# Kernel optimization log

Measured on AMD Instinct MI355X. Metric: run time of the kernel, lower is better.

## Reference

```python
import jax, jax.numpy as jnp
import numpy as np

N_NODES = 100000


def _gcn_layer(x, src, dst, deg_inv_sqrt, W, b):
    # GCNConv: out = D^{-1/2} (A + I) D^{-1/2} X W + b  (symmetric norm, self-loops)
    xw = x @ W  # [N, out]
    norm = deg_inv_sqrt[src] * deg_inv_sqrt[dst]  # [E]
    msg = xw[src] * norm[:, None]  # [E, out] gathered messages
    agg = jax.ops.segment_sum(msg, dst, num_segments=N_NODES)
    # self-loop contribution: norm_ii = deg_inv_sqrt[i]^2
    agg = agg + (deg_inv_sqrt * deg_inv_sqrt)[:, None] * xw
    return agg + b


def setup_inputs() -> dict:
    key = jax.random.key(0)
    k1, k2, k3, k4, k5, k6 = jax.random.split(key, 6)
    F_IN, HID, OUT, E = 128, 256, 40, 1600000
    x = jax.random.normal(k1, (N_NODES, F_IN), dtype=jnp.float32)
    edge_index = jax.random.randint(k2, (2, E), 0, N_NODES, dtype=jnp.int64)
    s1 = 1.0 / np.sqrt(F_IN)
    s2 = 1.0 / np.sqrt(HID)
    W1 = jax.random.uniform(k3, (F_IN, HID), jnp.float32, -s1, s1)
    b1 = jnp.zeros((HID,), jnp.float32)
    W2 = jax.random.uniform(k4, (HID, OUT), jnp.float32, -s2, s2)
    b2 = jnp.zeros((OUT,), jnp.float32)
    return {"x": x, "edge_index": edge_index, "W1": W1, "b1": b1, "W2": W2, "b2": b2}


def reference(x, edge_index, W1, b1, W2, b2):
    src, dst = edge_index[0], edge_index[1]
    # degree with self-loops (GCNConv default add_self_loops=True)
    deg = jax.ops.segment_sum(jnp.ones_like(dst, dtype=x.dtype), dst, num_segments=N_NODES) + 1.0
    deg_inv_sqrt = jax.lax.rsqrt(deg)
    h = _gcn_layer(x, src, dst, deg_inv_sqrt, W1, b1)
    h = jax.nn.relu(h)
    # dropout is identity in eval mode
    h = _gcn_layer(h, src, dst, deg_inv_sqrt, W2, b2)
    return jax.nn.log_softmax(h, axis=1)
```

## Files before the change

### kernel.cpp

```cpp
#include <hip/hip_runtime.h>
#include <math.h>

typedef long long ll;
typedef unsigned int uint;
typedef __attribute__((ext_vector_type(8))) short bf16x8;
typedef __attribute__((ext_vector_type(4))) float f32x4;

#define FIN 128
#define HID 256
#define FOUT 40

__device__ __forceinline__ float bflo(uint u) { return __uint_as_float(u << 16); }
__device__ __forceinline__ float bfhi(uint u) { return __uint_as_float(u & 0xFFFF0000u); }
__device__ __forceinline__ unsigned short f2bf(float f) {
  uint u = __float_as_uint(f);
  u += 0x7FFFu + ((u >> 16) & 1u);
  return (unsigned short)(u >> 16);
}

__device__ __forceinline__ int edge_val(const void* ei, ll idx, int is64) {
  return is64 ? (int)((const ll*)ei)[idx] : ((const int*)ei)[idx];
}

__global__ void k_init(const unsigned* __restrict__ ei, int* __restrict__ flag,
                       int* __restrict__ cnt,
                       const float* __restrict__ W1, const float* __restrict__ W2,
                       unsigned short* __restrict__ w1p,
                       unsigned short* __restrict__ w2p, int n) {
  int i = blockIdx.x * 256 + threadIdx.x;
  if (i == 0)
    flag[0] = (ei[1] == 0u && ei[3] == 0u && ei[5] == 0u && ei[7] == 0u) ? 1 : 0;
  if (i < n) cnt[i] = 0;
  if (i < 32768) {
    int j = i & 7, g = (i >> 3) & 3, c = (i >> 5) & 255, s = i >> 13;
    int k = s * 32 + g * 8 + j;
    w1p[i] = f2bf(W1[(size_t)k * HID + c]);
  } else if (i < 32768 + 12288) {
    int i2 = i - 32768;
    int j = i2 & 7, g = (i2 >> 3) & 3, q = i2 >> 5;
    int c = q % 48, s = q / 48;
    int k = s * 32 + g * 8 + j;
    w2p[i2] = (c < FOUT) ? f2bf(W2[(size_t)k * FOUT + c]) : (unsigned short)0;
  }
}

__global__ void k_xcast(const float* __restrict__ x, unsigned short* __restrict__ xb,
                        int total8) {
  int i = blockIdx.x * 256 + threadIdx.x;
  if (i >= total8) return;
  const float4* p = (const float4*)x + (size_t)i * 2;
  float4 a = p[0], b = p[1];
  uint4 o;
  o.x = (uint)f2bf(a.x) | ((uint)f2bf(a.y) << 16);
  o.y = (uint)f2bf(a.z) | ((uint)f2bf(a.w) << 16);
  o.z = (uint)f2bf(b.x) | ((uint)f2bf(b.y) << 16);
  o.w = (uint)f2bf(b.z) | ((uint)f2bf(b.w) << 16);
  *(uint4*)(xb + (size_t)i * 8) = o;
}

__global__ void k_count(const void* __restrict__ ei, const int* __restrict__ flag,
                        int* __restrict__ cnt, ll E) {
  ll base = ((ll)blockIdx.x * 256 + threadIdx.x) * 4;
  if (base >= E) return;
  int is64 = flag[0];
  int m = (int)((E - base < 4) ? (E - base) : 4);
  int d[4];
  if (is64) {
    if (m == 4 && ((E + base) & 1) == 0) {
      longlong2 v0 = *(const longlong2*)((const ll*)ei + E + base);
      longlong2 v1 = *(const longlong2*)((const ll*)ei + E + base + 2);
      d[0] = (int)v0.x; d[1] = (int)v0.y; d[2] = (int)v1.x; d[3] = (int)v1.y;
    } else {
      for (int j = 0; j < m; ++j) d[j] = (int)((const ll*)ei)[E + base + j];
    }
  } else {
    if (m == 4 && ((E + base) & 3) == 0) {
      int4 v = *(const int4*)((const int*)ei + E + base);
      d[0] = v.x; d[1] = v.y; d[2] = v.z; d[3] = v.w;
    } else {
      for (int j = 0; j < m; ++j) d[j] = ((const int*)ei)[E + base + j];
    }
  }
  for (int j = 0; j < m; ++j) atomicAdd(&cnt[d[j]], 1);
}

__global__ __launch_bounds__(1024) void k_scan1(const int* __restrict__ cnt,
                                                int* __restrict__ row_off,
                                                int* __restrict__ blksums, int n) {
  __shared__ int sm[1024];
  int t = threadIdx.x;
  int base = blockIdx.x * 4096 + t * 4;
  int v0 = (base + 0 < n) ? cnt[base + 0] : 0;
  int v1 = (base + 1 < n) ? cnt[base + 1] : 0;
  int v2 = (base + 2 < n) ? cnt[base + 2] : 0;
  int v3 = (base + 3 < n) ? cnt[base + 3] : 0;
  int s = v0 + v1 + v2 + v3;
  sm[t] = s;
  __syncthreads();
  for (int off = 1; off < 1024; off <<= 1) {
    int u = (t >= off) ? sm[t - off] : 0;
    __syncthreads();
    sm[t] += u;
    __syncthreads();
  }
  int excl = sm[t] - s;
  if (base + 0 < n) row_off[base + 0] = excl;
  if (base + 1 < n) row_off[base + 1] = excl + v0;
  if (base + 2 < n) row_off[base + 2] = excl + v0 + v1;
  if (base + 3 < n) row_off[base + 3] = excl + v0 + v1 + v2;
  if (t == 1023) blksums[blockIdx.x] = sm[1023];
}

__global__ void k_scan2(int* __restrict__ blksums, int nb) {
  if (threadIdx.x == 0 && blockIdx.x == 0) {
    int acc = 0;
    for (int i = 0; i < nb; ++i) { int v = blksums[i]; blksums[i] = acc; acc += v; }
    blksums[nb] = acc;
  }
}

__global__ void k_scan3(int* __restrict__ row_off, int* __restrict__ cursor,
                        const int* __restrict__ blksums, float* __restrict__ dis,
                        int n, int nb) {
  int i = blockIdx.x * 1024 + threadIdx.x;
  if (i < n) {
    int c = cursor[i];
    int v = row_off[i] + blksums[i >> 12];
    row_off[i] = v;
    cursor[i] = v;
    dis[i] = rsqrtf((float)c + 1.0f);
  }
  if (i == 0) row_off[n] = blksums[nb];
}

__global__ void k_fill(const void* __restrict__ ei, const int* __restrict__ flag,
                       const float* __restrict__ dis, int* __restrict__ cursor,
                       int2* __restrict__ csr2, ll E) {
  ll e = (ll)blockIdx.x * 256 + threadIdx.x;
  if (e < E) {
    int is64 = flag[0];
    int src = edge_val(ei, e, is64);
    int dst = edge_val(ei, E + e, is64);
    float wsrc = dis[src];
    int pos = atomicAdd(&cursor[dst], 1);
    csr2[pos] = make_int2(src, __float_as_int(wsrc));
  }
}

__device__ __forceinline__ void acc8(float* a, uint4 r, float w) {
  a[0] += w * bflo(r.x); a[1] += w * bfhi(r.x);
  a[2] += w * bflo(r.y); a[3] += w * bfhi(r.y);
  a[4] += w * bflo(r.z); a[5] += w * bfhi(r.z);
  a[6] += w * bflo(r.w); a[7] += w * bfhi(r.w);
}

__global__ __launch_bounds__(256) void k_fused1(
    const unsigned short* __restrict__ xb, const int2* __restrict__ csr2,
    const int* __restrict__ row_off, const float* __restrict__ dis,
    const unsigned short* __restrict__ w1p, const float* __restrict__ b1,
    const unsigned short* __restrict__ w2p, unsigned short* __restrict__ xw2b,
    int n)
{
  __shared__ __align__(16) unsigned short xsb[16 * 136];
  __shared__ __align__(16) unsigned short hsb[16 * 264];

  int tid = threadIdx.x;
  int n0 = blockIdx.x * 16;
  int wv = tid >> 6, lane = tid & 63, qq = lane >> 4, l16 = lane & 15;
  int nl = wv * 4 + qq;
  int node = n0 + nl;

  float a[8] = {0, 0, 0, 0, 0, 0, 0, 0};
  if (node < n) {
    float di = dis[node];
    uint4 v = *((const uint4*)(xb + (size_t)node * FIN) + l16);
    acc8(a, v, di * di);
    int e0 = row_off[node], e1 = row_off[node + 1];
    int e = e0;
    for (; e + 4 <= e1; e += 4) {
      int2 c0 = csr2[e], c1 = csr2[e + 1], c2 = csr2[e + 2], c3 = csr2[e + 3];
      uint4 r0 = *((const uint4*)(xb + (size_t)c0.x * FIN) + l16);
      uint4 r1 = *((const uint4*)(xb + (size_t)c1.x * FIN) + l16);
      uint4 r2 = *((const uint4*)(xb + (size_t)c2.x * FIN) + l16);
      uint4 r3 = *((const uint4*)(xb + (size_t)c3.x * FIN) + l16);
      acc8(a, r0, di * __int_as_float(c0.y));
      acc8(a, r1, di * __int_as_float(c1.y));
      acc8(a, r2, di * __int_as_float(c2.y));
      acc8(a, r3, di * __int_as_float(c3.y));
    }
    for (; e < e1; ++e) {
      int2 c0 = csr2[e];
      uint4 r0 = *((const uint4*)(xb + (size_t)c0.x * FIN) + l16);
      acc8(a, r0, di * __int_as_float(c0.y));
    }
  }
  {
    uint4 pk;
    pk.x = (uint)f2bf(a[0]) | ((uint)f2bf(a[1]) << 16);
    pk.y = (uint)f2bf(a[2]) | ((uint)f2bf(a[3]) << 16);
    pk.z = (uint)f2bf(a[4]) | ((uint)f2bf(a[5]) << 16);
    pk.w = (uint)f2bf(a[6]) | ((uint)f2bf(a[7]) << 16);
    *(uint4*)(xsb + nl * 136 + l16 * 8) = pk;
  }
  __syncthreads();

  int mrow = lane & 15, g = lane >> 4;
  f32x4 acc1[4] = {{0,0,0,0},{0,0,0,0},{0,0,0,0},{0,0,0,0}};
  #pragma unroll
  for (int s = 0; s < 4; ++s) {
    bf16x8 av = *(const bf16x8*)(xsb + mrow * 136 + s * 32 + g * 8);
    #pragma unroll
    for (int t = 0; t < 4; ++t) {
      int c = wv * 64 + t * 16 + mrow;
      bf16x8 bv = *(const bf16x8*)(w1p + (((size_t)(s * 256 + c) * 4 + g) << 3));
      acc1[t] = __builtin_amdgcn_mfma_f32_16x16x32_bf16(av, bv, acc1[t], 0, 0, 0);
    }
  }
  #pragma unroll
  for (int t = 0; t < 4; ++t) {
    int c = wv * 64 + t * 16 + mrow;
    float bb = b1[c];
    #pragma unroll
    for (int r = 0; r < 4; ++r) {
      float v = fmaxf(acc1[t][r] + bb, 0.f);
      hsb[(g * 4 + r) * 264 + c] = f2bf(v);
    }
  }
  __syncthreads();

  if (wv < 3) {
    f32x4 acc2 = {0, 0, 0, 0};
    int c2 = wv * 16 + mrow;
    #pragma unroll
    for (int s = 0; s < 8; ++s) {
      bf16x8 av = *(const bf16x8*)(hsb + mrow * 264 + s * 32 + g * 8);
      bf16x8 bv = *(const bf16x8*)(w2p + (((size_t)(s * 48 + c2) * 4 + g) << 3));
      acc2 = __builtin_amdgcn_mfma_f32_16x16x32_bf16(av, bv, acc2, 0, 0, 0);
    }
    if (c2 < FOUT) {
      #pragma unroll
      for (int r = 0; r < 4; ++r) {
        int nodeg = n0 + g * 4 + r;
        if (nodeg < n) xw2b[((size_t)nodeg << 6) + c2] = f2bf(acc2[r]);
      }
    }
  }
}

__global__ __launch_bounds__(256) void k_layer2(
    const unsigned short* __restrict__ xw2b, const int2* __restrict__ csr2,
    const int* __restrict__ row_off, const float* __restrict__ dis,
    const float* __restrict__ b2, float* __restrict__ out, int n)
{
  int tid = threadIdx.x;
  int node = blockIdx.x * 16 + (tid >> 4);
  int l16 = tid & 15;
  if (node >= n) return;
  float di = dis[node];
  float a0 = 0.f, a1 = 0.f, a2 = 0.f, a3 = 0.f;
  {
    uint2 v = *((const uint2*)(xw2b + ((size_t)node << 6)) + l16);
    float w = di * di;
    a0 = w * bflo(v.x); a1 = w * bfhi(v.x);
    a2 = w * bflo(v.y); a3 = w * bfhi(v.y);
  }
  int e0 = row_off[node], e1 = row_off[node + 1];
  int e = e0;
  for (; e + 4 <= e1; e += 4) {
    int2 c0 = csr2[e], c1 = csr2[e + 1], c2 = csr2[e + 2], c3 = csr2[e + 3];
    uint2 r0 = *((const uint2*)(xw2b + ((size_t)c0.x << 6)) + l16);
    uint2 r1 = *((const uint2*)(xw2b + ((size_t)c1.x << 6)) + l16);
    uint2 r2 = *((const uint2*)(xw2b + ((size_t)c2.x << 6)) + l16);
    uint2 r3 = *((const uint2*)(xw2b + ((size_t)c3.x << 6)) + l16);
    float w0 = di * __int_as_float(c0.y), w1 = di * __int_as_float(c1.y);
    float w2 = di * __int_as_float(c2.y), w3 = di * __int_as_float(c3.y);
    a0 += w0 * bflo(r0.x); a1 += w0 * bfhi(r0.x); a2 += w0 * bflo(r0.y); a3 += w0 * bfhi(r0.y);
    a0 += w1 * bflo(r1.x); a1 += w1 * bfhi(r1.x); a2 += w1 * bflo(r1.y); a3 += w1 * bfhi(r1.y);
    a0 += w2 * bflo(r2.x); a1 += w2 * bfhi(r2.x); a2 += w2 * bflo(r2.y); a3 += w2 * bfhi(r2.y);
    a0 += w3 * bflo(r3.x); a1 += w3 * bfhi(r3.x); a2 += w3 * bflo(r3.y); a3 += w3 * bfhi(r3.y);
  }
  for (; e < e1; ++e) {
    int2 c0 = csr2[e];
    uint2 r0 = *((const uint2*)(xw2b + ((size_t)c0.x << 6)) + l16);
    float w0 = di * __int_as_float(c0.y);
    a0 += w0 * bflo(r0.x); a1 += w0 * bfhi(r0.x);
    a2 += w0 * bflo(r0.y); a3 += w0 * bfhi(r0.y);
  }
  bool act = (l16 < 10);
  float l0 = -INFINITY, l1 = -INFINITY, l2 = -INFINITY, l3 = -INFINITY;
  if (act) {
    float4 bv = *(const float4*)(b2 + l16 * 4);
    l0 = a0 + bv.x; l1 = a1 + bv.y; l2 = a2 + bv.z; l3 = a3 + bv.w;
  }
  float m = fmaxf(fmaxf(l0, l1), fmaxf(l2, l3));
  #pragma unroll
  for (int off = 8; off > 0; off >>= 1) m = fmaxf(m, __shfl_xor(m, off));
  float s = 0.f;
  if (act) s = expf(l0 - m) + expf(l1 - m) + expf(l2 - m) + expf(l3 - m);
  #pragma unroll
  for (int off = 8; off > 0; off >>= 1) s += __shfl_xor(s, off);
  if (act) {
    float ls = m + logf(s);
    float4 o = make_float4(l0 - ls, l1 - ls, l2 - ls, l3 - ls);
    *(float4*)(out + (size_t)node * FOUT + l16 * 4) = o;
  }
}

extern "C" void kernel_launch(void* const* d_in, const int* in_sizes, int n_in,
                              void* d_out, int out_size, void* d_ws, size_t ws_size,
                              hipStream_t stream) {
  const float* x  = (const float*)d_in[0];
  const void*  ei = d_in[1];
  const float* W1 = (const float*)d_in[2];
  const float* b1 = (const float*)d_in[3];
  const float* W2 = (const float*)d_in[4];
  const float* b2 = (const float*)d_in[5];
  float* out = (float*)d_out;

  int n = in_sizes[0] / FIN;
  ll  E = (ll)in_sizes[1] / 2;
  int nb = (n + 4095) / 4096;

  char* ws = (char*)d_ws;
  size_t off = 0;
  auto carve = [&](size_t bytes) -> char* {
    char* p = ws + off;
    off = (off + bytes + 255) & ~(size_t)255;
    return p;
  };
  int*   flag    = (int*)carve(16);
  int*   row_off = (int*)carve((size_t)(n + 1) * 4);
  int*   cursor  = (int*)carve((size_t)n * 4);
  int2*  csr2    = (int2*)carve((size_t)E * 8);
  int*   blksums = (int*)carve(64 * 4);
  float* dis     = (float*)carve((size_t)n * 4);
  unsigned short* xb   = (unsigned short*)carve((size_t)n * FIN * 2);
  unsigned short* w1p  = (unsigned short*)carve(32768 * 2);
  unsigned short* w2p  = (unsigned short*)carve(12288 * 2);
  unsigned short* xw2b = (unsigned short*)carve((size_t)n * 64 * 2);
  (void)n_in; (void)out_size; (void)ws_size;

  int gn256 = (n + 255) / 256;
  int gE256 = (int)((E + 255) / 256);
  int gE4   = (int)((E + 1023) / 1024);
  int gx8   = (n * FIN / 8 + 255) / 256;
  int gt16  = (n + 15) / 16;

  hipLaunchKernelGGL(k_init,  dim3(gn256), dim3(256), 0, stream,
                     (const unsigned*)ei, flag, cursor, W1, W2, w1p, w2p, n);
  hipLaunchKernelGGL(k_count, dim3(gE4), dim3(256), 0, stream, ei, flag, cursor, E);
  hipLaunchKernelGGL(k_scan1, dim3(nb), dim3(1024), 0, stream, cursor, row_off, blksums, n);
  hipLaunchKernelGGL(k_scan2, dim3(1), dim3(1), 0, stream, blksums, nb);
  hipLaunchKernelGGL(k_scan3, dim3((n + 1023) / 1024), dim3(1024), 0, stream,
                     row_off, cursor, blksums, dis, n, nb);
  hipLaunchKernelGGL(k_fill,  dim3(gE256), dim3(256), 0, stream,
                     ei, flag, dis, cursor, csr2, E);
  hipLaunchKernelGGL(k_xcast, dim3(gx8), dim3(256), 0, stream, x, xb, n * FIN / 8);
  hipLaunchKernelGGL(k_fused1, dim3(gt16), dim3(256), 0, stream,
                     xb, csr2, row_off, dis, w1p, b1, w2p, xw2b, n);
  hipLaunchKernelGGL(k_layer2, dim3(gt16), dim3(256), 0, stream,
                     xw2b, csr2, row_off, dis, b2, out, n);
}
```

Before: 323.5 us.

## Prescale features by D^-1/2, shrink CSR to int, partition atomics by destination range

Source-side normalization is folded into the features: x is scaled by dis during the bf16 cast, and the layer-1 output is scaled by dis before it is written. The aggregation loops therefore become plain sums over 4-byte source indices, unrolled by 8, instead of reading 8-byte (src, weight) pairs. Edge indices are first packed into an int2 pairs buffer, and the count and fill kernels split destinations into 8 ranges so that each block group issues atomics to a narrower region, which is meant to improve atomic locality. In exchange each count/fill kernel reads the whole pairs array 8 times, and there is an extra pairs buffer plus a change in bf16 rounding order.

```diff
diff --git a/kernel.cpp b/kernel.cpp
--- a/kernel.cpp
+++ b/kernel.cpp
@@ -9,6 +9,7 @@
 #define FIN 128
 #define HID 256
 #define FOUT 40
+#define NG 8
 
 __device__ __forceinline__ float bflo(uint u) { return __uint_as_float(u << 16); }
 __device__ __forceinline__ float bfhi(uint u) { return __uint_as_float(u & 0xFFFF0000u); }
@@ -18,18 +19,17 @@
   return (unsigned short)(u >> 16);
 }
 
-__device__ __forceinline__ int edge_val(const void* ei, ll idx, int is64) {
-  return is64 ? (int)((const ll*)ei)[idx] : ((const int*)ei)[idx];
-}
-
-__global__ void k_init(const unsigned* __restrict__ ei, int* __restrict__ flag,
-                       int* __restrict__ cnt,
-                       const float* __restrict__ W1, const float* __restrict__ W2,
-                       unsigned short* __restrict__ w1p,
-                       unsigned short* __restrict__ w2p, int n) {
+__device__ __forceinline__ int detect64(const uint* __restrict__ ei) {
+  return (ei[1] == 0u && ei[3] == 0u && ei[5] == 0u && ei[7] == 0u) ? 1 : 0;
+}
+
+__global__ __launch_bounds__(256) void k_init(
+    const void* __restrict__ ei, int* __restrict__ cnt,
+    const float* __restrict__ W1, const float* __restrict__ W2,
+    unsigned short* __restrict__ w1p, unsigned short* __restrict__ w2p,
+    int2* __restrict__ pairs, int n, ll E) {
   int i = blockIdx.x * 256 + threadIdx.x;
-  if (i == 0)
-    flag[0] = (ei[1] == 0u && ei[3] == 0u && ei[5] == 0u && ei[7] == 0u) ? 1 : 0;
+  int T = gridDim.x * 256;
   if (i < n) cnt[i] = 0;
   if (i < 32768) {
     int j = i & 7, g = (i >> 3) & 3, c = (i >> 5) & 255, s = i >> 13;
@@ -42,46 +42,52 @@
     int k = s * 32 + g * 8 + j;
     w2p[i2] = (c < FOUT) ? f2bf(W2[(size_t)k * FOUT + c]) : (unsigned short)0;
   }
-}
-
-__global__ void k_xcast(const float* __restrict__ x, unsigned short* __restrict__ xb,
-                        int total8) {
-  int i = blockIdx.x * 256 + threadIdx.x;
-  if (i >= total8) return;
-  const float4* p = (const float4*)x + (size_t)i * 2;
-  float4 a = p[0], b = p[1];
-  uint4 o;
-  o.x = (uint)f2bf(a.x) | ((uint)f2bf(a.y) << 16);
-  o.y = (uint)f2bf(a.z) | ((uint)f2bf(a.w) << 16);
-  o.z = (uint)f2bf(b.x) | ((uint)f2bf(b.y) << 16);
-  o.w = (uint)f2bf(b.z) | ((uint)f2bf(b.w) << 16);
-  *(uint4*)(xb + (size_t)i * 8) = o;
-}
-
-__global__ void k_count(const void* __restrict__ ei, const int* __restrict__ flag,
-                        int* __restrict__ cnt, ll E) {
-  ll base = ((ll)blockIdx.x * 256 + threadIdx.x) * 4;
-  if (base >= E) return;
-  int is64 = flag[0];
-  int m = (int)((E - base < 4) ? (E - base) : 4);
-  int d[4];
-  if (is64) {
-    if (m == 4 && ((E + base) & 1) == 0) {
-      longlong2 v0 = *(const longlong2*)((const ll*)ei + E + base);
-      longlong2 v1 = *(const longlong2*)((const ll*)ei + E + base + 2);
-      d[0] = (int)v0.x; d[1] = (int)v0.y; d[2] = (int)v1.x; d[3] = (int)v1.y;
+  int is64 = detect64((const uint*)ei);
+  for (ll base = (ll)i * 4; base < E; base += (ll)T * 4) {
+    int m = (int)((E - base < 4) ? (E - base) : 4);
+    int s[4], d[4];
+    if (is64) {
+      if (m == 4) {
+        longlong2 a0 = *(const longlong2*)((const ll*)ei + base);
+        longlong2 a1 = *(const longlong2*)((const ll*)ei + base + 2);
+        longlong2 b0 = *(const longlong2*)((const ll*)ei + E + base);
+        longlong2 b1 = *(const longlong2*)((const ll*)ei + E + base + 2);
+        s[0]=(int)a0.x; s[1]=(int)a0.y; s[2]=(int)a1.x; s[3]=(int)a1.y;
+        d[0]=(int)b0.x; d[1]=(int)b0.y; d[2]=(int)b1.x; d[3]=(int)b1.y;
+      } else {
+        for (int j = 0; j < m; ++j) { s[j]=(int)((const ll*)ei)[base+j]; d[j]=(int)((const ll*)ei)[E+base+j]; }
+      }
     } else {
-      for (int j = 0; j < m; ++j) d[j] = (int)((const ll*)ei)[E + base + j];
-    }
-  } else {
-    if (m == 4 && ((E + base) & 3) == 0) {
-      int4 v = *(const int4*)((const int*)ei + E + base);
-      d[0] = v.x; d[1] = v.y; d[2] = v.z; d[3] = v.w;
+      if (m == 4) {
+        int4 a = *(const int4*)((const int*)ei + base);
+        int4 b = *(const int4*)((const int*)ei + E + base);
+        s[0]=a.x; s[1]=a.y; s[2]=a.z; s[3]=a.w;
+        d[0]=b.x; d[1]=b.y; d[2]=b.z; d[3]=b.w;
+      } else {
+        for (int j = 0; j < m; ++j) { s[j]=((const int*)ei)[base+j]; d[j]=((const int*)ei)[E+base+j]; }
+      }
+    }
+    for (int j = 0; j < m; ++j) pairs[base + j] = make_int2(s[j], d[j]);
+  }
+}
+
+__global__ __launch_bounds__(256) void k_count(
+    const int2* __restrict__ pairs, int* __restrict__ cnt, ll E, int range, int n) {
+  int g = blockIdx.x & (NG - 1);
+  int lo = g * range;
+  int hi = min(n, lo + range);
+  ll tig = (ll)(blockIdx.x >> 3) * 256 + threadIdx.x;
+  ll TIG = (ll)(gridDim.x >> 3) * 256;
+  for (ll i = tig * 2; i < E; i += TIG * 2) {
+    if (i + 1 < E) {
+      int4 p = *(const int4*)(pairs + i);
+      if (p.y >= lo && p.y < hi) atomicAdd(&cnt[p.y], 1);
+      if (p.w >= lo && p.w < hi) atomicAdd(&cnt[p.w], 1);
     } else {
-      for (int j = 0; j < m; ++j) d[j] = ((const int*)ei)[E + base + j];
-    }
-  }
-  for (int j = 0; j < m; ++j) atomicAdd(&cnt[d[j]], 1);
+      int2 p = pairs[i];
+      if (p.y >= lo && p.y < hi) atomicAdd(&cnt[p.y], 1);
+    }
+  }
 }
 
 __global__ __launch_bounds__(1024) void k_scan1(const int* __restrict__ cnt,
@@ -133,29 +139,51 @@
   if (i == 0) row_off[n] = blksums[nb];
 }
 
-__global__ void k_fill(const void* __restrict__ ei, const int* __restrict__ flag,
-                       const float* __restrict__ dis, int* __restrict__ cursor,
-                       int2* __restrict__ csr2, ll E) {
-  ll e = (ll)blockIdx.x * 256 + threadIdx.x;
-  if (e < E) {
-    int is64 = flag[0];
-    int src = edge_val(ei, e, is64);
-    int dst = edge_val(ei, E + e, is64);
-    float wsrc = dis[src];
-    int pos = atomicAdd(&cursor[dst], 1);
-    csr2[pos] = make_int2(src, __float_as_int(wsrc));
-  }
-}
-
-__device__ __forceinline__ void acc8(float* a, uint4 r, float w) {
-  a[0] += w * bflo(r.x); a[1] += w * bfhi(r.x);
-  a[2] += w * bflo(r.y); a[3] += w * bfhi(r.y);
-  a[4] += w * bflo(r.z); a[5] += w * bfhi(r.z);
-  a[6] += w * bflo(r.w); a[7] += w * bfhi(r.w);
+__global__ __launch_bounds__(256) void k_fill(
+    const int2* __restrict__ pairs, int* __restrict__ cursor,
+    int* __restrict__ csr, ll E, int range, int n) {
+  int g = blockIdx.x & (NG - 1);
+  int lo = g * range;
+  int hi = min(n, lo + range);
+  ll tig = (ll)(blockIdx.x >> 3) * 256 + threadIdx.x;
+  ll TIG = (ll)(gridDim.x >> 3) * 256;
+  for (ll i = tig * 2; i < E; i += TIG * 2) {
+    if (i + 1 < E) {
+      int4 p = *(const int4*)(pairs + i);
+      if (p.y >= lo && p.y < hi) { int pos = atomicAdd(&cursor[p.y], 1); csr[pos] = p.x; }
+      if (p.w >= lo && p.w < hi) { int pos = atomicAdd(&cursor[p.w], 1); csr[pos] = p.z; }
+    } else {
+      int2 p = pairs[i];
+      if (p.y >= lo && p.y < hi) { int pos = atomicAdd(&cursor[p.y], 1); csr[pos] = p.x; }
+    }
+  }
+}
+
+__global__ __launch_bounds__(256) void k_xcast(
+    const float* __restrict__ x, const float* __restrict__ dis,
+    unsigned short* __restrict__ xb, int total8) {
+  int i = blockIdx.x * 256 + threadIdx.x;
+  if (i >= total8) return;
+  float w = dis[i >> 4];
+  const float4* p = (const float4*)x + (size_t)i * 2;
+  float4 a = p[0], b = p[1];
+  uint4 o;
+  o.x = (uint)f2bf(w * a.x) | ((uint)f2bf(w * a.y) << 16);
+  o.y = (uint)f2bf(w * a.z) | ((uint)f2bf(w * a.w) << 16);
+  o.z = (uint)f2bf(w * b.x) | ((uint)f2bf(w * b.y) << 16);
+  o.w = (uint)f2bf(w * b.z) | ((uint)f2bf(w * b.w) << 16);
+  *(uint4*)(xb + (size_t)i * 8) = o;
+}
+
+__device__ __forceinline__ void add8(float* a, uint4 r) {
+  a[0] += bflo(r.x); a[1] += bfhi(r.x);
+  a[2] += bflo(r.y); a[3] += bfhi(r.y);
+  a[4] += bflo(r.z); a[5] += bfhi(r.z);
+  a[6] += bflo(r.w); a[7] += bfhi(r.w);
 }
 
 __global__ __launch_bounds__(256) void k_fused1(
-    const unsigned short* __restrict__ xb, const int2* __restrict__ csr2,
+    const unsigned short* __restrict__ xb, const int* __restrict__ csr,
     const int* __restrict__ row_off, const float* __restrict__ dis,
     const unsigned short* __restrict__ w1p, const float* __restrict__ b1,
     const unsigned short* __restrict__ w2p, unsigned short* __restrict__ xw2b,
@@ -171,35 +199,38 @@
   int node = n0 + nl;
 
   float a[8] = {0, 0, 0, 0, 0, 0, 0, 0};
+  float di = 0.f;
   if (node < n) {
-    float di = dis[node];
+    di = dis[node];
     uint4 v = *((const uint4*)(xb + (size_t)node * FIN) + l16);
-    acc8(a, v, di * di);
+    add8(a, v);
     int e0 = row_off[node], e1 = row_off[node + 1];
     int e = e0;
-    for (; e + 4 <= e1; e += 4) {
-      int2 c0 = csr2[e], c1 = csr2[e + 1], c2 = csr2[e + 2], c3 = csr2[e + 3];
-      uint4 r0 = *((const uint4*)(xb + (size_t)c0.x * FIN) + l16);
-      uint4 r1 = *((const uint4*)(xb + (size_t)c1.x * FIN) + l16);
-      uint4 r2 = *((const uint4*)(xb + (size_t)c2.x * FIN) + l16);
-      uint4 r3 = *((const uint4*)(xb + (size_t)c3.x * FIN) + l16);
-      acc8(a, r0, di * __int_as_float(c0.y));
-      acc8(a, r1, di * __int_as_float(c1.y));
-      acc8(a, r2, di * __int_as_float(c2.y));
-      acc8(a, r3, di * __int_as_float(c3.y));
+    for (; e + 8 <= e1; e += 8) {
+      int s0 = csr[e],     s1 = csr[e + 1], s2 = csr[e + 2], s3 = csr[e + 3];
+      int s4 = csr[e + 4], s5 = csr[e + 5], s6 = csr[e + 6], s7 = csr[e + 7];
+      uint4 r0 = *((const uint4*)(xb + (size_t)s0 * FIN) + l16);
+      uint4 r1 = *((const uint4*)(xb + (size_t)s1 * FIN) + l16);
+      uint4 r2 = *((const uint4*)(xb + (size_t)s2 * FIN) + l16);
+      uint4 r3 = *((const uint4*)(xb + (size_t)s3 * FIN) + l16);
+      uint4 r4 = *((const uint4*)(xb + (size_t)s4 * FIN) + l16);
+      uint4 r5 = *((const uint4*)(xb + (size_t)s5 * FIN) + l16);
+      uint4 r6 = *((const uint4*)(xb + (size_t)s6 * FIN) + l16);
+      uint4 r7 = *((const uint4*)(xb + (size_t)s7 * FIN) + l16);
+      add8(a, r0); add8(a, r1); add8(a, r2); add8(a, r3);
+      add8(a, r4); add8(a, r5); add8(a, r6); add8(a, r7);
     }
     for (; e < e1; ++e) {
-      int2 c0 = csr2[e];
-      uint4 r0 = *((const uint4*)(xb + (size_t)c0.x * FIN) + l16);
-      acc8(a, r0, di * __int_as_float(c0.y));
+      uint4 r0 = *((const uint4*)(xb + (size_t)csr[e] * FIN) + l16);
+      add8(a, r0);
     }
   }
   {
     uint4 pk;
-    pk.x = (uint)f2bf(a[0]) | ((uint)f2bf(a[1]) << 16);
-    pk.y = (uint)f2bf(a[2]) | ((uint)f2bf(a[3]) << 16);
-    pk.z = (uint)f2bf(a[4]) | ((uint)f2bf(a[5]) << 16);
-    pk.w = (uint)f2bf(a[6]) | ((uint)f2bf(a[7]) << 16);
+    pk.x = (uint)f2bf(di * a[0]) | ((uint)f2bf(di * a[1]) << 16);
+    pk.y = (uint)f2bf(di * a[2]) | ((uint)f2bf(di * a[3]) << 16);
+    pk.z = (uint)f2bf(di * a[4]) | ((uint)f2bf(di * a[5]) << 16);
+    pk.w = (uint)f2bf(di * a[6]) | ((uint)f2bf(di * a[7]) << 16);
     *(uint4*)(xsb + nl * 136 + l16 * 8) = pk;
   }
   __syncthreads();
@@ -241,14 +272,15 @@
       #pragma unroll
       for (int r = 0; r < 4; ++r) {
         int nodeg = n0 + g * 4 + r;
-        if (nodeg < n) xw2b[((size_t)nodeg << 6) + c2] = f2bf(acc2[r]);
+        if (nodeg < n)
+          xw2b[((size_t)nodeg << 6) + c2] = f2bf(acc2[r] * dis[nodeg]);
       }
     }
   }
 }
 
 __global__ __launch_bounds__(256) void k_layer2(
-    const unsigned short* __restrict__ xw2b, const int2* __restrict__ csr2,
+    const unsigned short* __restrict__ xw2b, const int* __restrict__ csr,
     const int* __restrict__ row_off, const float* __restrict__ dis,
     const float* __restrict__ b2, float* __restrict__ out, int n)
 {
@@ -257,40 +289,43 @@
   int l16 = tid & 15;
   if (node >= n) return;
   float di = dis[node];
-  float a0 = 0.f, a1 = 0.f, a2 = 0.f, a3 = 0.f;
+  float a0, a1, a2, a3;
   {
     uint2 v = *((const uint2*)(xw2b + ((size_t)node << 6)) + l16);
-    float w = di * di;
-    a0 = w * bflo(v.x); a1 = w * bfhi(v.x);
-    a2 = w * bflo(v.y); a3 = w * bfhi(v.y);
+    a0 = bflo(v.x); a1 = bfhi(v.x); a2 = bflo(v.y); a3 = bfhi(v.y);
   }
   int e0 = row_off[node], e1 = row_off[node + 1];
   int e = e0;
-  for (; e + 4 <= e1; e += 4) {
-    int2 c0 = csr2[e], c1 = csr2[e + 1], c2 = csr2[e + 2], c3 = csr2[e + 3];
-    uint2 r0 = *((const uint2*)(xw2b + ((size_t)c0.x << 6)) + l16);
-    uint2 r1 = *((const uint2*)(xw2b + ((size_t)c1.x << 6)) + l16);
-    uint2 r2 = *((const uint2*)(xw2b + ((size_t)c2.x << 6)) + l16);
-    uint2 r3 = *((const uint2*)(xw2b + ((size_t)c3.x << 6)) + l16);
-    float w0 = di * __int_as_float(c0.y), w1 = di * __int_as_float(c1.y);
-    float w2 = di * __int_as_float(c2.y), w3 = di * __int_as_float(c3.y);
-    a0 += w0 * bflo(r0.x); a1 += w0 * bfhi(r0.x); a2 += w0 * bflo(r0.y); a3 += w0 * bfhi(r0.y);
-    a0 += w1 * bflo(r1.x); a1 += w1 * bfhi(r1.x); a2 += w1 * bflo(r1.y); a3 += w1 * bfhi(r1.y);
-    a0 += w2 * bflo(r2.x); a1 += w2 * bfhi(r2.x); a2 += w2 * bflo(r2.y); a3 += w2 * bfhi(r2.y);
-    a0 += w3 * bflo(r3.x); a1 += w3 * bfhi(r3.x); a2 += w3 * bflo(r3.y); a3 += w3 * bfhi(r3.y);
+  for (; e + 8 <= e1; e += 8) {
+    int s0 = csr[e],     s1 = csr[e + 1], s2 = csr[e + 2], s3 = csr[e + 3];
+    int s4 = csr[e + 4], s5 = csr[e + 5], s6 = csr[e + 6], s7 = csr[e + 7];
+    uint2 r0 = *((const uint2*)(xw2b + ((size_t)s0 << 6)) + l16);
+    uint2 r1 = *((const uint2*)(xw2b + ((size_t)s1 << 6)) + l16);
+    uint2 r2 = *((const uint2*)(xw2b + ((size_t)s2 << 6)) + l16);
+    uint2 r3 = *((const uint2*)(xw2b + ((size_t)s3 << 6)) + l16);
+    uint2 r4 = *((const uint2*)(xw2b + ((size_t)s4 << 6)) + l16);
+    uint2 r5 = *((const uint2*)(xw2b + ((size_t)s5 << 6)) + l16);
+    uint2 r6 = *((const uint2*)(xw2b + ((size_t)s6 << 6)) + l16);
+    uint2 r7 = *((const uint2*)(xw2b + ((size_t)s7 << 6)) + l16);
+    a0 += bflo(r0.x); a1 += bfhi(r0.x); a2 += bflo(r0.y); a3 += bfhi(r0.y);
+    a0 += bflo(r1.x); a1 += bfhi(r1.x); a2 += bflo(r1.y); a3 += bfhi(r1.y);
+    a0 += bflo(r2.x); a1 += bfhi(r2.x); a2 += bflo(r2.y); a3 += bfhi(r2.y);
+    a0 += bflo(r3.x); a1 += bfhi(r3.x); a2 += bflo(r3.y); a3 += bfhi(r3.y);
+    a0 += bflo(r4.x); a1 += bfhi(r4.x); a2 += bflo(r4.y); a3 += bfhi(r4.y);
+    a0 += bflo(r5.x); a1 += bfhi(r5.x); a2 += bflo(r5.y); a3 += bfhi(r5.y);
+    a0 += bflo(r6.x); a1 += bfhi(r6.x); a2 += bflo(r6.y); a3 += bfhi(r6.y);
+    a0 += bflo(r7.x); a1 += bfhi(r7.x); a2 += bflo(r7.y); a3 += bfhi(r7.y);
   }
   for (; e < e1; ++e) {
-    int2 c0 = csr2[e];
-    uint2 r0 = *((const uint2*)(xw2b + ((size_t)c0.x << 6)) + l16);
-    float w0 = di * __int_as_float(c0.y);
-    a0 += w0 * bflo(r0.x); a1 += w0 * bfhi(r0.x);
-    a2 += w0 * bflo(r0.y); a3 += w0 * bfhi(r0.y);
+    uint2 r0 = *((const uint2*)(xw2b + ((size_t)csr[e] << 6)) + l16);
+    a0 += bflo(r0.x); a1 += bfhi(r0.x); a2 += bflo(r0.y); a3 += bfhi(r0.y);
   }
   bool act = (l16 < 10);
   float l0 = -INFINITY, l1 = -INFINITY, l2 = -INFINITY, l3 = -INFINITY;
   if (act) {
     float4 bv = *(const float4*)(b2 + l16 * 4);
-    l0 = a0 + bv.x; l1 = a1 + bv.y; l2 = a2 + bv.z; l3 = a3 + bv.w;
+    l0 = di * a0 + bv.x; l1 = di * a1 + bv.y;
+    l2 = di * a2 + bv.z; l3 = di * a3 + bv.w;
   }
   float m = fmaxf(fmaxf(l0, l1), fmaxf(l2, l3));
   #pragma unroll
@@ -320,6 +355,7 @@
   int n = in_sizes[0] / FIN;
   ll  E = (ll)in_sizes[1] / 2;
   int nb = (n + 4095) / 4096;
+  int range = (n + NG - 1) / NG;
 
   char* ws = (char*)d_ws;
   size_t off = 0;
@@ -328,10 +364,10 @@
     off = (off + bytes + 255) & ~(size_t)255;
     return p;
   };
-  int*   flag    = (int*)carve(16);
   int*   row_off = (int*)carve((size_t)(n + 1) * 4);
   int*   cursor  = (int*)carve((size_t)n * 4);
-  int2*  csr2    = (int2*)carve((size_t)E * 8);
+  int2*  pairs   = (int2*)carve((size_t)E * 8);
+  int*   csr     = (int*)carve((size_t)E * 4);
   int*   blksums = (int*)carve(64 * 4);
   float* dis     = (float*)carve((size_t)n * 4);
   unsigned short* xb   = (unsigned short*)carve((size_t)n * FIN * 2);
@@ -341,23 +377,20 @@
   (void)n_in; (void)out_size; (void)ws_size;
 
   int gn256 = (n + 255) / 256;
-  int gE256 = (int)((E + 255) / 256);
-  int gE4   = (int)((E + 1023) / 1024);
   int gx8   = (n * FIN / 8 + 255) / 256;
   int gt16  = (n + 15) / 16;
 
   hipLaunchKernelGGL(k_init,  dim3(gn256), dim3(256), 0, stream,
-                     (const unsigned*)ei, flag, cursor, W1, W2, w1p, w2p, n);
-  hipLaunchKernelGGL(k_count, dim3(gE4), dim3(256), 0, stream, ei, flag, cursor, E);
+                     ei, cursor, W1, W2, w1p, w2p, pairs, n, E);
+  hipLaunchKernelGGL(k_count, dim3(512), dim3(256), 0, stream, pairs, cursor, E, range, n);
   hipLaunchKernelGGL(k_scan1, dim3(nb), dim3(1024), 0, stream, cursor, row_off, blksums, n);
   hipLaunchKernelGGL(k_scan2, dim3(1), dim3(1), 0, stream, blksums, nb);
   hipLaunchKernelGGL(k_scan3, dim3((n + 1023) / 1024), dim3(1024), 0, stream,
                      row_off, cursor, blksums, dis, n, nb);
-  hipLaunchKernelGGL(k_fill,  dim3(gE256), dim3(256), 0, stream,
-                     ei, flag, dis, cursor, csr2, E);
-  hipLaunchKernelGGL(k_xcast, dim3(gx8), dim3(256), 0, stream, x, xb, n * FIN / 8);
+  hipLaunchKernelGGL(k_fill,  dim3(512), dim3(256), 0, stream, pairs, cursor, csr, E, range, n);
+  hipLaunchKernelGGL(k_xcast, dim3(gx8), dim3(256), 0, stream, x, dis, xb, n * FIN / 8);
   hipLaunchKernelGGL(k_fused1, dim3(gt16), dim3(256), 0, stream,
-                     xb, csr2, row_off, dis, w1p, b1, w2p, xw2b, n);
+                     xb, csr, row_off, dis, w1p, b1, w2p, xw2b, n);
   hipLaunchKernelGGL(k_layer2, dim3(gt16), dim3(256), 0, stream,
-                     xw2b, csr2, row_off, dis, b2, out, n);
-}
+                     xw2b, csr, row_off, dis, b2, out, n);
+}
```

Result: faster. 313.9 us (-3.0%).
